# Optimization experiments

Hardware: AMD Instinct MI355X
Metric: run time of the kernel (lower is better)

## Reference

```python
import jax, jax.numpy as jnp
import numpy as np

B, L, D = 32, 2048, 128
SCALE = 1.0 / float(np.sqrt(D))  # scale = 1/sqrt(dim_K) per docstring


def setup_inputs() -> dict:
    key = jax.random.key(0)
    kq, kk, kv, kb = jax.random.split(key, 4)
    return {
        "Q": jax.random.normal(kq, (B, L, D), dtype=jnp.float32),
        "K": jax.random.normal(kk, (B, L, D), dtype=jnp.float32),
        "V": jax.random.normal(kv, (B, L, D), dtype=jnp.float32),
        "bias": jax.random.normal(kb, (L, L), dtype=jnp.float32),
    }


def reference(Q, K, V, bias):
    # scores = Q @ K^T + bias (bias broadcast over batch), then scale, softmax, @ V
    scores = jnp.einsum("bqd,bkd->bqk", Q, K) + bias[None, :, :]
    attn = jax.nn.softmax(scores * SCALE, axis=-1)  # [B, L, L]
    context = jnp.einsum("bqk,bkd->bqd", attn, V)   # [B, L, D]
    return (context, attn[0])
```

## Files before the change

kernel.cpp:

```cpp
#include <hip/hip_runtime.h>
#include <cstdint>
#include <cstddef>

#define L_ 2048
#define D_ 128
#define B_ 32
#define NT_ 32

static constexpr float SCALE = 0.08838834764831845f;
static constexpr float LOG2E = 1.4426950408889634f;
static constexpr float MH_ = 12.0f * LOG2E;

typedef __bf16 bf16x8 __attribute__((ext_vector_type(8)));
typedef __bf16 bf16x4 __attribute__((ext_vector_type(4)));
typedef float  f32x4  __attribute__((ext_vector_type(4)));
typedef int    i32x4  __attribute__((ext_vector_type(4)));

typedef const __attribute__((address_space(1))) uint32_t* gas_t;
typedef __attribute__((address_space(3))) uint32_t*       las_t;

__device__ __forceinline__ void dma16(const void* g, void* l) {
  __builtin_amdgcn_global_load_lds((gas_t)g, (las_t)l, 16, 0, 0);
}

__device__ __forceinline__ int cperm(int r) {
  return (r & 32) | (((r >> 3) & 1) << 4) | (((r >> 2) & 1) << 3)
       | (((r >> 4) & 1) << 2) | (r & 3);
}

__global__ __launch_bounds__(256) void prep_kv(
    const float* __restrict__ K, const float* __restrict__ V,
    __bf16* __restrict__ gK, __bf16* __restrict__ gVt)
{
  const int b   = blockIdx.x >> 5;
  const int kt  = blockIdx.x & 31;
  const int tid = threadIdx.x;
  const size_t tile = ((size_t)b * NT_ + kt) * 8192;

#pragma unroll
  for (int i = 0; i < 4; ++i) {
    const int g  = tid + i * 256;
    const int r  = g >> 4;
    const int c  = g & 15;
    const int d0 = (c ^ (r & 7)) * 8;
    const float* src = K + ((size_t)b * L_ + kt * 64 + r) * D_ + d0;
    float4 a = *(const float4*)src;
    float4 e = *(const float4*)(src + 4);
    bf16x8 f;
    f[0]=(__bf16)a.x; f[1]=(__bf16)a.y; f[2]=(__bf16)a.z; f[3]=(__bf16)a.w;
    f[4]=(__bf16)e.x; f[5]=(__bf16)e.y; f[6]=(__bf16)e.z; f[7]=(__bf16)e.w;
    *(bf16x8*)((char*)(gK + tile) + r * 256 + c * 16) = f;
  }

  __shared__ alignas(16) __bf16 Vt[8192];
  char* vb = (char*)Vt;
  const int vr     = tid & 63;
  const int vc     = cperm(vr);
  const int vdbase = (tid >> 6) * 32;
  const float* vrow = V + ((size_t)b * L_ + kt * 64 + vr) * D_ + vdbase;
#pragma unroll
  for (int c = 0; c < 8; ++c) {
    float4 v4 = *(const float4*)(vrow + c * 4);
    const int d0 = vdbase + c * 4;
    float vv[4] = {v4.x, v4.y, v4.z, v4.w};
#pragma unroll
    for (int jj = 0; jj < 4; ++jj) {
      const int d = d0 + jj;
      *(__bf16*)(vb + d * 128 + ((vc * 2) ^ ((d & 7) << 4))) = (__bf16)vv[jj];
    }
  }
  __syncthreads();
#pragma unroll
  for (int i = 0; i < 4; ++i) {
    const int off = (tid + i * 256) * 16;
    *(i32x4*)((char*)(gVt + tile) + off) = *(const i32x4*)(vb + off);
  }
}

template<int MODE>
__global__ __launch_bounds__(512, 4) void attn_fwd(
    const float* __restrict__ Q, const float* __restrict__ K,
    const float* __restrict__ V, const float* __restrict__ bias,
    const __bf16* __restrict__ gK, const __bf16* __restrict__ gVt,
    float* __restrict__ ctx, float* __restrict__ attn0)
{
  const int id   = blockIdx.x;
  const int idx  = id >> 3;
  const int b    = (id & 7) * 4 + (idx >> 4);
  const int qblk = idx & 15;

  const int tid  = threadIdx.x;
  const int wave = tid >> 6;
  const int lane = tid & 63;
  const int lg   = lane >> 4;
  const int lr   = lane & 15;

  const int qbase = qblk * 128 + wave * 16;

  __shared__ alignas(16) __bf16 Ksh[8192];
  __shared__ alignas(16) __bf16 Vtsh[8192];
  const char* kb = (const char*)Ksh;
  const char* vb = (const char*)Vtsh;

  bf16x8 qf[4];
  {
    const float* qrow = Q + ((size_t)b * L_ + (qbase + lr)) * D_;
#pragma unroll
    for (int kc = 0; kc < 4; ++kc) {
      const int d0 = kc * 32 + lg * 8;
      float4 a = *(const float4*)(qrow + d0);
      float4 c = *(const float4*)(qrow + d0 + 4);
      bf16x8 f;
      f[0] = (__bf16)(a.x * SCALE); f[1] = (__bf16)(a.y * SCALE);
      f[2] = (__bf16)(a.z * SCALE); f[3] = (__bf16)(a.w * SCALE);
      f[4] = (__bf16)(c.x * SCALE); f[5] = (__bf16)(c.y * SCALE);
      f[6] = (__bf16)(c.z * SCALE); f[7] = (__bf16)(c.w * SCALE);
      qf[kc] = f;
    }
  }

  f32x4 Oacc[8];
#pragma unroll
  for (int i = 0; i < 8; ++i) Oacc[i] = (f32x4){0.f, 0.f, 0.f, 0.f};
  float lp = 0.f;

  auto stage_dma = [&](int kt) {
    const char* gk = (const char*)(gK + ((size_t)b * NT_ + kt) * 8192);
    const char* gv = (const char*)(gVt + ((size_t)b * NT_ + kt) * 8192);
#pragma unroll
    for (int i = 0; i < 2; ++i) {
      const int off = (wave * 2 + i) * 1024;
      dma16(gk + off + lane * 16, (char*)Ksh + off);
      dma16(gv + off + lane * 16, (char*)Vtsh + off);
    }
  };

  if constexpr (MODE >= 1) stage_dma(0);

  for (int kt = 0; kt < NT_; ++kt) {
    const int kvbase = kt * 64;

    if constexpr (MODE == 0) {
#pragma unroll
      for (int it = 0; it < 4; ++it) {
        const int g  = tid + it * 512;
        const int r  = g >> 5;
        const int d0 = (g & 31) * 4;
        const size_t src = ((size_t)b * L_ + (kvbase + r)) * D_ + d0;
        float4 kv4 = *(const float4*)(K + src);
        bf16x4 k4 = {(__bf16)kv4.x, (__bf16)kv4.y, (__bf16)kv4.z, (__bf16)kv4.w};
        *(bf16x4*)((char*)Ksh + r * 256 + ((d0 * 2) ^ ((r & 7) << 4))) = k4;
      }
      {
        const int vr = tid & 63;
        const int vc = cperm(vr);
        const int vdbase = (tid >> 6) * 16;
        const float* vrow = V + ((size_t)b * L_ + (kvbase + vr)) * D_ + vdbase;
#pragma unroll
        for (int c = 0; c < 4; ++c) {
          float4 v4 = *(const float4*)(vrow + c * 4);
          const int d0 = vdbase + c * 4;
          float vv[4] = {v4.x, v4.y, v4.z, v4.w};
#pragma unroll
          for (int jj = 0; jj < 4; ++jj) {
            const int d = d0 + jj;
            *(__bf16*)((char*)Vtsh + d * 128 + ((vc * 2) ^ ((d & 7) << 4))) = (__bf16)vv[jj];
          }
        }
      }
    }
    __syncthreads();

    float4 bf4[4];
    {
      const float* bp = bias + (size_t)(qbase + lr) * L_ + kvbase + lg * 4;
#pragma unroll
      for (int t = 0; t < 4; ++t) bf4[t] = *(const float4*)(bp + t * 16);
    }

    f32x4 Sacc[4];
#pragma unroll
    for (int t = 0; t < 4; ++t) Sacc[t] = (f32x4){0.f, 0.f, 0.f, 0.f};
    __builtin_amdgcn_s_setprio(1);
#pragma unroll
    for (int t = 0; t < 4; ++t) {
      const int r   = t * 16 + lr;
      const int swz = (r & 7) << 4;
#pragma unroll
      for (int kc = 0; kc < 4; ++kc) {
        const int d0 = kc * 32 + lg * 8;
        bf16x8 kf = *(const bf16x8*)(kb + r * 256 + ((d0 * 2) ^ swz));
        Sacc[t] = __builtin_amdgcn_mfma_f32_16x16x32_bf16(kf, qf[kc], Sacc[t], 0, 0, 0);
      }
    }
    __builtin_amdgcn_s_setprio(0);

    float zz[4][4];
#pragma unroll
    for (int t = 0; t < 4; ++t) {
      zz[t][0] = fmaf(bf4[t].x, SCALE, Sacc[t][0]);
      zz[t][1] = fmaf(bf4[t].y, SCALE, Sacc[t][1]);
      zz[t][2] = fmaf(bf4[t].z, SCALE, Sacc[t][2]);
      zz[t][3] = fmaf(bf4[t].w, SCALE, Sacc[t][3]);
    }
    if (b == 0) {
      float* ap = attn0 + (size_t)(qbase + lr) * L_ + kvbase + lg * 4;
#pragma unroll
      for (int t = 0; t < 4; ++t)
        *(float4*)(ap + t * 16) = make_float4(zz[t][0], zz[t][1], zz[t][2], zz[t][3]);
    }

    bf16x4 pbf[4];
#pragma unroll
    for (int t = 0; t < 4; ++t) {
#pragma unroll
      for (int j = 0; j < 4; ++j) {
        const float p = exp2f(fmaf(zz[t][j], LOG2E, -MH_));
        lp += p;
        pbf[t][j] = (__bf16)p;
      }
    }

    __builtin_amdgcn_s_setprio(1);
#pragma unroll
    for (int kc2 = 0; kc2 < 2; ++kc2) {
      bf16x8 pa;
      pa[0] = pbf[kc2 * 2][0];     pa[1] = pbf[kc2 * 2][1];
      pa[2] = pbf[kc2 * 2][2];     pa[3] = pbf[kc2 * 2][3];
      pa[4] = pbf[kc2 * 2 + 1][0]; pa[5] = pbf[kc2 * 2 + 1][1];
      pa[6] = pbf[kc2 * 2 + 1][2]; pa[7] = pbf[kc2 * 2 + 1][3];
      const int c0 = kc2 * 32;
#pragma unroll
      for (int dt = 0; dt < 8; ++dt) {
        const int d = dt * 16 + lr;
        bf16x8 vf = *(const bf16x8*)(vb + d * 128 + (((c0 + lg * 8) * 2) ^ ((d & 7) << 4)));
        Oacc[dt] = __builtin_amdgcn_mfma_f32_16x16x32_bf16(pa, vf, Oacc[dt], 0, 0, 0);
      }
    }
    __builtin_amdgcn_s_setprio(0);

    __syncthreads();
    if constexpr (MODE >= 1) {
      if (kt + 1 < NT_) stage_dma(kt + 1);
    }
  }

  float ls = lp;
  ls += __shfl_xor(ls, 16);
  ls += __shfl_xor(ls, 32);
  const float linv = 1.f / ls;
  float invR[4];
#pragma unroll
  for (int j = 0; j < 4; ++j)
    invR[j] = __shfl(linv, (lane & 0x30) | (lg * 4 + j));
#pragma unroll
  for (int dt = 0; dt < 8; ++dt) {
    const int d = dt * 16 + lr;
#pragma unroll
    for (int j = 0; j < 4; ++j) {
      const int q = qbase + lg * 4 + j;
      ctx[((size_t)b * L_ + q) * D_ + d] = Oacc[dt][j] * invR[j];
    }
  }
}

__global__ __launch_bounds__(256) void softmax_rows(float* __restrict__ attn0)
{
  const int row  = blockIdx.x;
  float* p = attn0 + (size_t)row * L_;
  const int tid  = threadIdx.x;
  const int wave = tid >> 6;
  const int lane = tid & 63;
  __shared__ float red[8];

  float4 a = ((const float4*)p)[tid];
  float4 c = ((const float4*)p)[tid + 256];
  float v[8] = {a.x, a.y, a.z, a.w, c.x, c.y, c.z, c.w};

  float mx = v[0];
#pragma unroll
  for (int i = 1; i < 8; ++i) mx = fmaxf(mx, v[i]);
#pragma unroll
  for (int msk = 1; msk < 64; msk <<= 1) mx = fmaxf(mx, __shfl_xor(mx, msk));
  if (lane == 0) red[wave] = mx;
  __syncthreads();
  mx = fmaxf(fmaxf(red[0], red[1]), fmaxf(red[2], red[3]));

  float e[8];
  float s = 0.f;
#pragma unroll
  for (int i = 0; i < 8; ++i) { e[i] = exp2f((v[i] - mx) * LOG2E); s += e[i]; }
#pragma unroll
  for (int msk = 1; msk < 64; msk <<= 1) s += __shfl_xor(s, msk);
  if (lane == 0) red[4 + wave] = s;
  __syncthreads();
  s = red[4] + red[5] + red[6] + red[7];
  const float inv = 1.f / s;

  float4 o0 = {e[0] * inv, e[1] * inv, e[2] * inv, e[3] * inv};
  float4 o1 = {e[4] * inv, e[5] * inv, e[6] * inv, e[7] * inv};
  ((float4*)p)[tid]       = o0;
  ((float4*)p)[tid + 256] = o1;
}

extern "C" void kernel_launch(void* const* d_in, const int* in_sizes, int n_in,
                              void* d_out, int out_size, void* d_ws, size_t ws_size,
                              hipStream_t stream) {
  const float* Q    = (const float*)d_in[0];
  const float* K    = (const float*)d_in[1];
  const float* V    = (const float*)d_in[2];
  const float* bias = (const float*)d_in[3];
  float* ctx   = (float*)d_out;
  float* attn0 = ctx + (size_t)B_ * L_ * D_;

  const size_t kvElems = (size_t)B_ * L_ * D_;
  const size_t needKV  = 2 * kvElems * sizeof(__bf16);

  __bf16* gK  = (__bf16*)d_ws;
  __bf16* gVt = gK + kvElems;

  if (ws_size >= needKV) {
    prep_kv<<<dim3(B_ * NT_), 256, 0, stream>>>(K, V, gK, gVt);
    attn_fwd<1><<<dim3(512), 512, 0, stream>>>(Q, K, V, bias, gK, gVt, ctx, attn0);
  } else {
    attn_fwd<0><<<dim3(512), 512, 0, stream>>>(Q, K, V, bias, nullptr, nullptr, ctx, attn0);
  }
  softmax_rows<<<L_, 256, 0, stream>>>(attn0);
}
```

Measured before the change: 148.1 us.

## Double-buffer K/V LDS tiles and split row-sum accumulators

In DMA mode the K and V^T shared-memory tiles are now double-buffered. The next tile's global-to-LDS copy is issued at the top of each iteration into the other buffer, so it overlaps the current tile's MFMA work, and each iteration needs one barrier instead of two. The softmax row-sum accumulation is also split into four independent partial sums, shortening the serial add dependency chain. LDS use doubles, which may lower occupancy. Nothing waits explicitly for the async DMA, so correctness depends on the barrier also covering completion of the global_load_lds transfers.

```diff
diff --git a/kernel.cpp b/kernel.cpp
--- a/kernel.cpp
+++ b/kernel.cpp
@@ -97,10 +97,9 @@
 
   const int qbase = qblk * 128 + wave * 16;
 
-  __shared__ alignas(16) __bf16 Ksh[8192];
-  __shared__ alignas(16) __bf16 Vtsh[8192];
-  const char* kb = (const char*)Ksh;
-  const char* vb = (const char*)Vtsh;
+  constexpr int NBUF = (MODE >= 1) ? 2 : 1;
+  __shared__ alignas(16) __bf16 Ksh[NBUF * 8192];
+  __shared__ alignas(16) __bf16 Vtsh[NBUF * 8192];
 
   bf16x8 qf[4];
   {
@@ -122,25 +121,33 @@
   f32x4 Oacc[8];
 #pragma unroll
   for (int i = 0; i < 8; ++i) Oacc[i] = (f32x4){0.f, 0.f, 0.f, 0.f};
-  float lp = 0.f;
-
-  auto stage_dma = [&](int kt) {
+  float lpA = 0.f, lpB = 0.f, lpC = 0.f, lpD = 0.f;
+
+  auto stage_dma = [&](int kt, int sel) {
     const char* gk = (const char*)(gK + ((size_t)b * NT_ + kt) * 8192);
     const char* gv = (const char*)(gVt + ((size_t)b * NT_ + kt) * 8192);
+    char* kdst = (char*)Ksh + sel * 16384;
+    char* vdst = (char*)Vtsh + sel * 16384;
 #pragma unroll
     for (int i = 0; i < 2; ++i) {
       const int off = (wave * 2 + i) * 1024;
-      dma16(gk + off + lane * 16, (char*)Ksh + off);
-      dma16(gv + off + lane * 16, (char*)Vtsh + off);
+      dma16(gk + off + lane * 16, kdst + off);
+      dma16(gv + off + lane * 16, vdst + off);
     }
   };
 
-  if constexpr (MODE >= 1) stage_dma(0);
+  if constexpr (MODE >= 1) stage_dma(0, 0);
 
   for (int kt = 0; kt < NT_; ++kt) {
     const int kvbase = kt * 64;
-
-    if constexpr (MODE == 0) {
+    const int cur = (MODE >= 1) ? (kt & 1) : 0;
+    const char* kb = (const char*)Ksh + cur * 16384;
+    const char* vb = (const char*)Vtsh + cur * 16384;
+
+    if constexpr (MODE >= 1) {
+      __syncthreads();
+      if (kt + 1 < NT_) stage_dma(kt + 1, cur ^ 1);
+    } else {
 #pragma unroll
       for (int it = 0; it < 4; ++it) {
         const int g  = tid + it * 512;
@@ -168,8 +175,8 @@
           }
         }
       }
-    }
-    __syncthreads();
+      __syncthreads();
+    }
 
     float4 bf4[4];
     {
@@ -213,12 +220,16 @@
     bf16x4 pbf[4];
 #pragma unroll
     for (int t = 0; t < 4; ++t) {
-#pragma unroll
-      for (int j = 0; j < 4; ++j) {
-        const float p = exp2f(fmaf(zz[t][j], LOG2E, -MH_));
-        lp += p;
-        pbf[t][j] = (__bf16)p;
-      }
+      float ps0 = exp2f(fmaf(zz[t][0], LOG2E, -MH_));
+      float ps1 = exp2f(fmaf(zz[t][1], LOG2E, -MH_));
+      float ps2 = exp2f(fmaf(zz[t][2], LOG2E, -MH_));
+      float ps3 = exp2f(fmaf(zz[t][3], LOG2E, -MH_));
+      if (t == 0) lpA += (ps0 + ps1) + (ps2 + ps3);
+      if (t == 1) lpB += (ps0 + ps1) + (ps2 + ps3);
+      if (t == 2) lpC += (ps0 + ps1) + (ps2 + ps3);
+      if (t == 3) lpD += (ps0 + ps1) + (ps2 + ps3);
+      pbf[t][0] = (__bf16)ps0; pbf[t][1] = (__bf16)ps1;
+      pbf[t][2] = (__bf16)ps2; pbf[t][3] = (__bf16)ps3;
     }
 
     __builtin_amdgcn_s_setprio(1);
@@ -239,13 +250,10 @@
     }
     __builtin_amdgcn_s_setprio(0);
 
-    __syncthreads();
-    if constexpr (MODE >= 1) {
-      if (kt + 1 < NT_) stage_dma(kt + 1);
-    }
-  }
-
-  float ls = lp;
+    if constexpr (MODE == 0) __syncthreads();
+  }
+
+  float ls = (lpA + lpB) + (lpC + lpD);
   ls += __shfl_xor(ls, 16);
   ls += __shfl_xor(ls, 32);
   const float linv = 1.f / ls;
```

Result: no change. 148.3 us (+0.1%).
